# Kernel tuning notes

Measured on AMD Instinct MI355X. Metric: run time of the kernel, lower is better.

Reference implementation:

```python
import jax, jax.numpy as jnp
import numpy as np

D_MODEL = 128
NUM_HEADS = 8
DEPTH = D_MODEL // NUM_HEADS
NEG = -1e9


def _dense_params(key, d_in, d_out):
    kw, kb = jax.random.split(key)
    # Glorot-uniform like keras Dense default
    lim = np.sqrt(6.0 / (d_in + d_out))
    w = jax.random.uniform(kw, (d_in, d_out), jnp.float32, -lim, lim)
    b = jnp.zeros((d_out,), jnp.float32)
    return w, b


def setup_inputs() -> dict:
    key = jax.random.key(0)
    ks = jax.random.split(key, 16)
    B, N, M, d = 256, 128, 128, D_MODEL
    inp = {
        'x_self': jax.random.normal(ks[0], (B, N, d), jnp.float32),
        'adj_self': jax.random.randint(ks[1], (B, N, N), 0, 2, jnp.int32),
        'mask_self': jnp.ones((B, N), jnp.int32),
        'x_cross': jax.random.normal(ks[2], (B, M, d), jnp.float32),
        'mask_cross': jnp.ones((B, M), jnp.int32),
    }
    names = ['wq_s', 'wk_s', 'wv_s', 'wo_s', 'wq_c', 'wk_c', 'wv_c', 'wo_c']
    for i, nm in enumerate(names):
        w, b = _dense_params(ks[3 + i], d, d)
        inp[nm] = w
        inp['b' + nm[1:]] = b
    wg, bg = _dense_params(ks[12], 3 * d, d)
    inp['wg'] = wg
    inp['bg'] = bg
    return inp


def _split_heads(x):
    B, N, _ = x.shape
    return x.reshape(B, N, NUM_HEADS, DEPTH).transpose(0, 2, 1, 3)  # [B,H,N,depth]


def _merge_heads(x):
    B, H, N, Dp = x.shape
    return x.transpose(0, 2, 1, 3).reshape(B, N, H * Dp)


def _attention(q, k, v, mask, adj=None):
    # q,k,v: [B,H,Nq,depth]; mask: [B,Nk]; adj: [B,Nq,Nk] or None
    logits = jnp.einsum('bhqd,bhkd->bhqk', q, k) / jnp.sqrt(jnp.float32(DEPTH))
    if adj is not None:
        logits = logits + ((1.0 - adj.astype(jnp.float32)) * NEG)[:, None, :, :]
    logits = logits + ((1.0 - mask.astype(jnp.float32)) * NEG)[:, None, None, :]
    w = jax.nn.softmax(logits, axis=-1)
    return jnp.einsum('bhqk,bhkd->bhqd', w, v)


def reference(x_self, adj_self, mask_self, x_cross, mask_cross,
              wq_s, bq_s, wk_s, bk_s, wv_s, bv_s, wo_s, bo_s,
              wq_c, bq_c, wk_c, bk_c, wv_c, bv_c, wo_c, bo_c,
              wg, bg):
    # Self attention (adjacency + padding mask)
    q_s = _split_heads(x_self @ wq_s + bq_s)
    k_s = _split_heads(x_self @ wk_s + bk_s)
    v_s = _split_heads(x_self @ wv_s + bv_s)
    out_s = _merge_heads(_attention(q_s, k_s, v_s, mask_self, adj_self)) @ wo_s + bo_s
    # Cross attention (padding mask only); dropout inactive at inference
    q_c = _split_heads(x_self @ wq_c + bq_c)
    k_c = _split_heads(x_cross @ wk_c + bk_c)
    v_c = _split_heads(x_cross @ wv_c + bv_c)
    out_c = _merge_heads(_attention(q_c, k_c, v_c, mask_cross)) @ wo_c + bo_c
    # Sigmoid gate fusion
    gate = jax.nn.sigmoid(jnp.concatenate([x_self, out_s, out_c], axis=-1) @ wg + bg)
    return (1.0 - gate) * out_s + gate * out_c
```

## Files before the change

### kernel.cpp

```cpp
#include <hip/hip_runtime.h>
#include <hip/hip_bf16.h>

typedef _Float16 f16_t;
typedef __attribute__((ext_vector_type(8))) _Float16 f16x8;
typedef __attribute__((ext_vector_type(4))) float f32x4;
typedef __attribute__((ext_vector_type(16))) float f32x16;

__global__ __launch_bounds__(256) void transpose_w(
    const float* w0, const float* w1, const float* w2, const float* w3,
    const float* w4, const float* w5, const float* w6, const float* w7,
    const float* wg, f16_t* wt)
{
  __shared__ float t[128][129];
  const int b = blockIdx.x;
  const int tid = threadIdx.x;
  const float* src;
  f16_t* dst;
  int ostride;
  switch (b) {
    case 0: src = w0; break;  case 1: src = w1; break;
    case 2: src = w2; break;  case 3: src = w3; break;
    case 4: src = w4; break;  case 5: src = w5; break;
    case 6: src = w6; break;  case 7: src = w7; break;
    default: src = wg + (size_t)(b - 8) * 16384; break;
  }
  if (b < 8) { dst = wt + (size_t)b * 16384; ostride = 128; }
  else       { dst = wt + 8 * 16384 + (b - 8) * 128; ostride = 384; }

#pragma unroll
  for (int i = 0; i < 64; ++i) {
    const int idx = tid + i * 256;
    const int r = idx >> 7, c = idx & 127;
    t[c][r] = src[idx];
  }
  __syncthreads();
#pragma unroll
  for (int i = 0; i < 64; ++i) {
    const int idx = tid + i * 256;
    const int c = idx >> 7, r = idx & 127;
    dst[(size_t)c * ostride + r] = (f16_t)t[c][r];
  }
}

template <int NW>
__global__ __launch_bounds__(256) void projN_kernel(
    const float* __restrict__ A, const f16_t* __restrict__ WT,
    const float* __restrict__ bias0, f16_t* __restrict__ Y0,
    const float* __restrict__ bias1, f16_t* __restrict__ Y1,
    const float* __restrict__ bias2, f16_t* __restrict__ Y2,
    const float* __restrict__ bias3, f16_t* __restrict__ Y3)
{
  const int tid = threadIdx.x;
  const int wv = tid >> 6;
  const int ln = tid & 63;
  const int l15 = ln & 15;
  const int g = ln >> 4;
  const size_t arow = (size_t)blockIdx.x * 64 + wv * 16 + l15;

  f32x4 acc[NW][8];
#pragma unroll
  for (int i = 0; i < NW; ++i)
#pragma unroll
    for (int nt = 0; nt < 8; ++nt) acc[i][nt] = (f32x4){0.f, 0.f, 0.f, 0.f};

#pragma unroll
  for (int kt = 0; kt < 4; ++kt) {
    const float* ap = A + arow * 128 + kt * 32 + g * 8;
    float4 v0 = *(const float4*)ap;
    float4 v1 = *(const float4*)(ap + 4);
    f16x8 a;
    a[0] = (f16_t)v0.x; a[1] = (f16_t)v0.y; a[2] = (f16_t)v0.z; a[3] = (f16_t)v0.w;
    a[4] = (f16_t)v1.x; a[5] = (f16_t)v1.y; a[6] = (f16_t)v1.z; a[7] = (f16_t)v1.w;
#pragma unroll
    for (int i = 0; i < NW; ++i) {
#pragma unroll
      for (int nt = 0; nt < 8; ++nt) {
        f16x8 b = *(const f16x8*)(WT + (size_t)i * 16384 +
                                  (size_t)(nt * 16 + l15) * 128 + kt * 32 + g * 8);
        acc[i][nt] = __builtin_amdgcn_mfma_f32_16x16x32_f16(a, b, acc[i][nt], 0, 0, 0);
      }
    }
  }

  const size_t orow0 = (size_t)blockIdx.x * 64 + wv * 16 + g * 4;
#pragma unroll
  for (int i = 0; i < NW; ++i) {
    const float* bp = (i == 0) ? bias0 : (i == 1) ? bias1 : (i == 2) ? bias2 : bias3;
    f16_t* Y = (i == 0) ? Y0 : (i == 1) ? Y1 : (i == 2) ? Y2 : Y3;
#pragma unroll
    for (int nt = 0; nt < 8; ++nt) {
      const int col = nt * 16 + l15;
      const float bv = bp[col];
#pragma unroll
      for (int r = 0; r < 4; ++r)
        Y[(orow0 + r) * 128 + col] = (f16_t)(acc[i][nt][r] + bv);
    }
  }
}

template <bool HAS_ADJ>
__global__ __launch_bounds__(256) void attn3_kernel(
    const f16_t* __restrict__ Q, const f16_t* __restrict__ K,
    const f16_t* __restrict__ V, const int* __restrict__ adj,
    const int* __restrict__ mask, f16_t* __restrict__ O)
{
  __shared__ __align__(16) f16_t Qh[128 * 24];
  __shared__ __align__(16) f16_t Kh[128 * 24];
  __shared__ __align__(16) f16_t Vt[16 * 136];
  __shared__ __align__(16) f16_t Pl[128 * 128];
  __shared__ float larr[128];
  __shared__ unsigned mw[4];
  __shared__ unsigned adjw[HAS_ADJ ? 128 * 4 : 4];

  const int bid = blockIdx.x;
  const int h = bid >> 8;
  const int bb = bid & 255;
  const int tid = threadIdx.x;
  const size_t base = (size_t)bb * 16384 + h * 16;

  {
    const int r = tid >> 1, hf = tid & 1;
    f16x8 qv = *(const f16x8*)(Q + base + (size_t)r * 128 + hf * 8);
    *(f16x8*)&Qh[r * 24 + hf * 8] = qv;
    f16x8 kv = *(const f16x8*)(K + base + (size_t)r * 128 + hf * 8);
    *(f16x8*)&Kh[r * 24 + hf * 8] = kv;
    f16x8 vv = *(const f16x8*)(V + base + (size_t)r * 128 + hf * 8);
#pragma unroll
    for (int j = 0; j < 8; ++j) Vt[(hf * 8 + j) * 136 + r] = vv[j];
  }
  if (tid < 128) {
    unsigned long long bm = __ballot(mask[bb * 128 + tid] != 0);
    if ((tid & 63) == 0) {
      mw[(tid >> 6) * 2 + 0] = (unsigned)bm;
      mw[(tid >> 6) * 2 + 1] = (unsigned)(bm >> 32);
    }
  }
  if (HAS_ADJ) {
    const int r = tid >> 1, hf = tid & 1;
    const int4* ap = (const int4*)(adj + ((size_t)bb * 128 + r) * 128 + hf * 64);
    unsigned w0 = 0, w1 = 0;
#pragma unroll
    for (int i = 0; i < 8; ++i) {
      int4 a = ap[i];
      unsigned m4 = (a.x != 0 ? 1u : 0u) | (a.y != 0 ? 2u : 0u) |
                    (a.z != 0 ? 4u : 0u) | (a.w != 0 ? 8u : 0u);
      w0 |= m4 << (i * 4);
    }
#pragma unroll
    for (int i = 8; i < 16; ++i) {
      int4 a = ap[i];
      unsigned m4 = (a.x != 0 ? 1u : 0u) | (a.y != 0 ? 2u : 0u) |
                    (a.z != 0 ? 4u : 0u) | (a.w != 0 ? 8u : 0u);
      w1 |= m4 << ((i - 8) * 4);
    }
    adjw[r * 4 + hf * 2 + 0] = w0;
    adjw[r * 4 + hf * 2 + 1] = w1;
  }
  __syncthreads();

  const int ln = tid & 63;
  const int wv = tid >> 6;
  const int l31 = ln & 31;
  const int hh = ln >> 5;
  const int q = wv * 32 + l31;

  f32x16 zero16;
#pragma unroll
  for (int j = 0; j < 16; ++j) zero16[j] = 0.f;
  const f16x8 bq = *(const f16x8*)&Qh[q * 24 + hh * 8];
  f32x16 st[4];
#pragma unroll
  for (int kt = 0; kt < 4; ++kt) {
    const f16x8 ak = *(const f16x8*)&Kh[(kt * 32 + l31) * 24 + hh * 8];
    st[kt] = __builtin_amdgcn_mfma_f32_32x32x16_f16(ak, bq, zero16, 0, 0, 0);
  }

  unsigned aw[4];
#pragma unroll
  for (int kt = 0; kt < 4; ++kt)
    aw[kt] = HAS_ADJ ? (adjw[q * 4 + kt] & mw[kt]) : mw[kt];

  const int swz = (q & 7) << 4;
  float l = 0.f;
#pragma unroll
  for (int kt = 0; kt < 4; ++kt) {
#pragma unroll
    for (int r2 = 0; r2 < 8; ++r2) {
      const int r = r2 * 2;
      const int koff = (r & 3) + 8 * (r >> 2) + 4 * hh;
      float e0 = __expf(st[kt][r]     * 0.25f - 8.f);
      float e1 = __expf(st[kt][r + 1] * 0.25f - 8.f);
      float p0 = ((aw[kt] >> koff) & 1u) ? e0 : 0.f;
      float p1 = ((aw[kt] >> (koff + 1)) & 1u) ? e1 : 0.f;
      l += p0 + p1;
      unsigned short u0 = __builtin_bit_cast(unsigned short, (f16_t)p0);
      unsigned short u1 = __builtin_bit_cast(unsigned short, (f16_t)p1);
      unsigned pk = (unsigned)u0 | ((unsigned)u1 << 16);
      const int key = kt * 32 + koff;
      *(unsigned*)((char*)Pl + q * 256 + ((key * 2) ^ swz)) = pk;
    }
  }
  l += __shfl_xor(l, 32);
  if (hh == 0) larr[q] = l;
  __syncthreads();

  const int l15 = ln & 15;
  const int g4 = ln >> 4;
  const int qa0 = wv * 32 + l15;
  const int qa1 = qa0 + 16;
  const int swz0 = (qa0 & 7) << 4;
  const int swz1 = (qa1 & 7) << 4;
  f32x4 o0 = (f32x4){0.f, 0.f, 0.f, 0.f};
  f32x4 o1 = (f32x4){0.f, 0.f, 0.f, 0.f};
#pragma unroll
  for (int kt = 0; kt < 4; ++kt) {
    const f16x8 bv = *(const f16x8*)&Vt[l15 * 136 + kt * 32 + g4 * 8];
    const f16x8 p0 = *(const f16x8*)((char*)Pl + qa0 * 256 + ((kt * 64 + g4 * 16) ^ swz0));
    const f16x8 p1 = *(const f16x8*)((char*)Pl + qa1 * 256 + ((kt * 64 + g4 * 16) ^ swz1));
    o0 = __builtin_amdgcn_mfma_f32_16x16x32_f16(p0, bv, o0, 0, 0, 0);
    o1 = __builtin_amdgcn_mfma_f32_16x16x32_f16(p1, bv, o1, 0, 0, 0);
  }
#pragma unroll
  for (int rr = 0; rr < 4; ++rr) {
    const int q0 = wv * 32 + g4 * 4 + rr;
    const int q1 = q0 + 16;
    const float i0 = 1.f / larr[q0];
    const float i1 = 1.f / larr[q1];
    O[base + (size_t)q0 * 128 + l15] = (f16_t)(o0[rr] * i0);
    O[base + (size_t)q1 * 128 + l15] = (f16_t)(o1[rr] * i1);
  }
}

__global__ __launch_bounds__(256) void outgate_kernel(
    const f16_t* __restrict__ AS, const f16_t* __restrict__ AC,
    const float* __restrict__ X, const f16_t* __restrict__ WT,
    const float* __restrict__ bos, const float* __restrict__ boc,
    const float* __restrict__ bgv, float* __restrict__ OUT)
{
  __shared__ __align__(16) f16_t OSl[64 * 136];
  __shared__ __align__(16) f16_t OCl[64 * 136];
  const int tid = threadIdx.x;
  const int wv = tid >> 6;
  const int ln = tid & 63;
  const int l15 = ln & 15;
  const int g = ln >> 4;
  const size_t arow = (size_t)blockIdx.x * 64 + wv * 16 + l15;
  const f16_t* WoS = WT + 6 * 16384;
  const f16_t* WoC = WT + 7 * 16384;
  const f16_t* Wg  = WT + 8 * 16384;

  f32x4 accS[8], accC[8], accG[8];
#pragma unroll
  for (int nt = 0; nt < 8; ++nt) {
    accS[nt] = (f32x4){0.f, 0.f, 0.f, 0.f};
    accC[nt] = (f32x4){0.f, 0.f, 0.f, 0.f};
    accG[nt] = (f32x4){0.f, 0.f, 0.f, 0.f};
  }

#pragma unroll
  for (int kt = 0; kt < 4; ++kt) {
    f16x8 aS = *(const f16x8*)(AS + arow * 128 + kt * 32 + g * 8);
    f16x8 aC = *(const f16x8*)(AC + arow * 128 + kt * 32 + g * 8);
#pragma unroll
    for (int nt = 0; nt < 8; ++nt) {
      f16x8 bS = *(const f16x8*)(WoS + (size_t)(nt * 16 + l15) * 128 + kt * 32 + g * 8);
      f16x8 bC = *(const f16x8*)(WoC + (size_t)(nt * 16 + l15) * 128 + kt * 32 + g * 8);
      accS[nt] = __builtin_amdgcn_mfma_f32_16x16x32_f16(aS, bS, accS[nt], 0, 0, 0);
      accC[nt] = __builtin_amdgcn_mfma_f32_16x16x32_f16(aC, bC, accC[nt], 0, 0, 0);
    }
  }
  const int lrow0 = wv * 16 + g * 4;
#pragma unroll
  for (int nt = 0; nt < 8; ++nt) {
    const int col = nt * 16 + l15;
    const float bS = bos[col], bC = boc[col];
#pragma unroll
    for (int r = 0; r < 4; ++r) {
      accS[nt][r] += bS;
      accC[nt][r] += bC;
      OSl[(lrow0 + r) * 136 + col] = (f16_t)accS[nt][r];
      OCl[(lrow0 + r) * 136 + col] = (f16_t)accC[nt][r];
    }
  }
  __syncthreads();

#pragma unroll
  for (int kt = 0; kt < 12; ++kt) {
    f16x8 a;
    if (kt < 4) {
      const float* ap = X + arow * 128 + kt * 32 + g * 8;
      float4 v0 = *(const float4*)ap;
      float4 v1 = *(const float4*)(ap + 4);
      a[0] = (f16_t)v0.x; a[1] = (f16_t)v0.y; a[2] = (f16_t)v0.z; a[3] = (f16_t)v0.w;
      a[4] = (f16_t)v1.x; a[5] = (f16_t)v1.y; a[6] = (f16_t)v1.z; a[7] = (f16_t)v1.w;
    } else if (kt < 8) {
      a = *(const f16x8*)&OSl[(wv * 16 + l15) * 136 + (kt - 4) * 32 + g * 8];
    } else {
      a = *(const f16x8*)&OCl[(wv * 16 + l15) * 136 + (kt - 8) * 32 + g * 8];
    }
#pragma unroll
    for (int nt = 0; nt < 8; ++nt) {
      f16x8 b = *(const f16x8*)(Wg + (size_t)(nt * 16 + l15) * 384 + kt * 32 + g * 8);
      accG[nt] = __builtin_amdgcn_mfma_f32_16x16x32_f16(a, b, accG[nt], 0, 0, 0);
    }
  }

  const size_t orow0 = (size_t)blockIdx.x * 64 + wv * 16 + g * 4;
#pragma unroll
  for (int nt = 0; nt < 8; ++nt) {
    const int col = nt * 16 + l15;
    const float bgc = bgv[col];
#pragma unroll
    for (int r = 0; r < 4; ++r) {
      const float gv = 1.f / (1.f + __expf(-(accG[nt][r] + bgc)));
      OUT[(orow0 + r) * 128 + col] = (1.f - gv) * accS[nt][r] + gv * accC[nt][r];
    }
  }
}

extern "C" void kernel_launch(void* const* d_in, const int* in_sizes, int n_in,
                              void* d_out, int out_size, void* d_ws, size_t ws_size,
                              hipStream_t stream)
{
  const float* x_self  = (const float*)d_in[0];
  const int*   adj     = (const int*)d_in[1];
  const int*   mask_s  = (const int*)d_in[2];
  const float* x_cross = (const float*)d_in[3];
  const int*   mask_c  = (const int*)d_in[4];
  const float* wq_s = (const float*)d_in[5];
  const float* bq_s = (const float*)d_in[6];
  const float* wk_s = (const float*)d_in[7];
  const float* bk_s = (const float*)d_in[8];
  const float* wv_s = (const float*)d_in[9];
  const float* bv_s = (const float*)d_in[10];
  const float* wo_s = (const float*)d_in[11];
  const float* bo_s = (const float*)d_in[12];
  const float* wq_c = (const float*)d_in[13];
  const float* bq_c = (const float*)d_in[14];
  const float* wk_c = (const float*)d_in[15];
  const float* bk_c = (const float*)d_in[16];
  const float* wv_c = (const float*)d_in[17];
  const float* bv_c = (const float*)d_in[18];
  const float* wo_c = (const float*)d_in[19];
  const float* bo_c = (const float*)d_in[20];
  const float* wg   = (const float*)d_in[21];
  const float* bg   = (const float*)d_in[22];
  float* out = (float*)d_out;

  const size_t SZ = (size_t)256 * 128 * 128;
  f16_t* w16 = (f16_t*)d_ws;
  f16_t* qs  = w16 + 0 * SZ;
  f16_t* ks  = w16 + 1 * SZ;
  f16_t* vs  = w16 + 2 * SZ;
  f16_t* qc  = w16 + 3 * SZ;
  f16_t* kc  = w16 + 4 * SZ;
  f16_t* vc  = w16 + 5 * SZ;
  f16_t* as_ = w16 + 6 * SZ;
  f16_t* ac_ = w16 + 7 * SZ;
  f16_t* WT  = w16 + 8 * SZ;

  transpose_w<<<11, 256, 0, stream>>>(wq_s, wk_s, wv_s, wq_c, wk_c, wv_c,
                                      wo_s, wo_c, wg, WT);
  projN_kernel<4><<<512, 256, 0, stream>>>(x_self, WT,
                                           bq_s, qs, bk_s, ks, bv_s, vs, bq_c, qc);
  projN_kernel<2><<<512, 256, 0, stream>>>(x_cross, WT + 4 * 16384,
                                           bk_c, kc, bv_c, vc, nullptr, nullptr,
                                           nullptr, nullptr);
  attn3_kernel<true><<<2048, 256, 0, stream>>>(qs, ks, vs, adj, mask_s, as_);
  attn3_kernel<false><<<2048, 256, 0, stream>>>(qc, kc, vc, nullptr, mask_c, ac_);
  outgate_kernel<<<512, 256, 0, stream>>>(as_, ac_, x_self, WT, bo_s, bo_c, bg, out);
}
```

Baseline: 162.8 us.

## Merge launches, precompose gate weights, and split projection tiles by columns

The two projection launches become one 2048-block launch and the two attention launches become one 4096-block launch, with a block-index switch selecting self or cross inputs. A prep kernel precomputes Wo_s·Wg and Wo_c·Wg plus a folded gate bias. This lets the output kernel compute the gate directly from the attention outputs, dropping the LDS staging, barrier and second GEMM pass. Projection and output tiles shrink to 32 rows with warps split across column halves, doubling the block count. The precomposed weights add fp16 rounding of a product matrix and some extra MFMA work per output block.

```diff
diff --git a/kernel.cpp b/kernel.cpp
--- a/kernel.cpp
+++ b/kernel.cpp
@@ -6,90 +6,133 @@
 typedef __attribute__((ext_vector_type(4))) float f32x4;
 typedef __attribute__((ext_vector_type(16))) float f32x16;
 
-__global__ __launch_bounds__(256) void transpose_w(
-    const float* w0, const float* w1, const float* w2, const float* w3,
-    const float* w4, const float* w5, const float* w6, const float* w7,
-    const float* wg, f16_t* wt)
-{
-  __shared__ float t[128][129];
+__device__ __forceinline__ f16x8 cvt8(const float* p) {
+  float4 v0 = *(const float4*)p;
+  float4 v1 = *(const float4*)(p + 4);
+  f16x8 a;
+  a[0] = (f16_t)v0.x; a[1] = (f16_t)v0.y; a[2] = (f16_t)v0.z; a[3] = (f16_t)v0.w;
+  a[4] = (f16_t)v1.x; a[5] = (f16_t)v1.y; a[6] = (f16_t)v1.z; a[7] = (f16_t)v1.w;
+  return a;
+}
+
+__global__ __launch_bounds__(256) void prep_kernel(
+    const float* wq_s, const float* wk_s, const float* wv_s,
+    const float* wq_c, const float* wk_c, const float* wv_c,
+    const float* wo_s, const float* wo_c, const float* wg,
+    const float* bos, const float* boc, const float* bgin,
+    f16_t* WT, float* bgp)
+{
   const int b = blockIdx.x;
   const int tid = threadIdx.x;
-  const float* src;
-  f16_t* dst;
-  int ostride;
-  switch (b) {
-    case 0: src = w0; break;  case 1: src = w1; break;
-    case 2: src = w2; break;  case 3: src = w3; break;
-    case 4: src = w4; break;  case 5: src = w5; break;
-    case 6: src = w6; break;  case 7: src = w7; break;
-    default: src = wg + (size_t)(b - 8) * 16384; break;
-  }
-  if (b < 8) { dst = wt + (size_t)b * 16384; ostride = 128; }
-  else       { dst = wt + 8 * 16384 + (b - 8) * 128; ostride = 384; }
-
-#pragma unroll
-  for (int i = 0; i < 64; ++i) {
-    const int idx = tid + i * 256;
-    const int r = idx >> 7, c = idx & 127;
-    t[c][r] = src[idx];
-  }
-  __syncthreads();
-#pragma unroll
-  for (int i = 0; i < 64; ++i) {
-    const int idx = tid + i * 256;
-    const int c = idx >> 7, r = idx & 127;
-    dst[(size_t)c * ostride + r] = (f16_t)t[c][r];
+  if (b < 11) {
+    __shared__ float t[128][129];
+    const float* src; f16_t* dst; int ostride;
+    switch (b) {
+      case 0: src = wq_s; break; case 1: src = wk_s; break;
+      case 2: src = wv_s; break; case 3: src = wq_c; break;
+      case 4: src = wk_c; break; case 5: src = wv_c; break;
+      case 6: src = wo_s; break; case 7: src = wo_c; break;
+      default: src = wg + (size_t)(b - 8) * 16384; break;
+    }
+    if (b < 8) { dst = WT + (size_t)b * 16384; ostride = 128; }
+    else       { dst = WT + 8 * 16384 + (b - 8) * 128; ostride = 384; }
+#pragma unroll
+    for (int i = 0; i < 64; ++i) {
+      const int idx = tid + i * 256;
+      t[idx & 127][idx >> 7] = src[idx];
+    }
+    __syncthreads();
+#pragma unroll
+    for (int i = 0; i < 64; ++i) {
+      const int idx = tid + i * 256;
+      const int c = idx >> 7, r = idx & 127;
+      dst[(size_t)c * ostride + r] = (f16_t)t[c][r];
+    }
+  } else if (b < 13) {
+    const int matsel = b - 11;
+    const float* wo = matsel ? wo_c : wo_s;
+    const int joff = 128 + matsel * 128;
+    f16_t* dst = WT + (size_t)(11 + matsel) * 16384;
+    const int wv = tid >> 6, ln = tid & 63, l15 = ln & 15, g = ln >> 4;
+    f32x4 acc[2][8];
+#pragma unroll
+    for (int mm = 0; mm < 2; ++mm)
+#pragma unroll
+      for (int nt = 0; nt < 8; ++nt) acc[mm][nt] = (f32x4){0.f, 0.f, 0.f, 0.f};
+#pragma unroll
+    for (int kt = 0; kt < 4; ++kt) {
+      f16x8 a[2];
+#pragma unroll
+      for (int mm = 0; mm < 2; ++mm) {
+        const int crow = wv * 32 + mm * 16 + l15;
+#pragma unroll
+        for (int jj = 0; jj < 8; ++jj)
+          a[mm][jj] = (f16_t)wg[(size_t)(joff + kt * 32 + g * 8 + jj) * 128 + crow];
+      }
+#pragma unroll
+      for (int nt = 0; nt < 8; ++nt) {
+        f16x8 bf = cvt8(wo + (size_t)(nt * 16 + l15) * 128 + kt * 32 + g * 8);
+        acc[0][nt] = __builtin_amdgcn_mfma_f32_16x16x32_f16(a[0], bf, acc[0][nt], 0, 0, 0);
+        acc[1][nt] = __builtin_amdgcn_mfma_f32_16x16x32_f16(a[1], bf, acc[1][nt], 0, 0, 0);
+      }
+    }
+#pragma unroll
+    for (int mm = 0; mm < 2; ++mm)
+#pragma unroll
+      for (int nt = 0; nt < 8; ++nt)
+#pragma unroll
+        for (int r = 0; r < 4; ++r) {
+          const int c = wv * 32 + mm * 16 + g * 4 + r;
+          dst[(size_t)c * 128 + nt * 16 + l15] = (f16_t)acc[mm][nt][r];
+        }
+  } else {
+    if (tid < 128) {
+      float acc = bgin[tid];
+      for (int j = 0; j < 128; ++j)
+        acc += bos[j] * wg[(size_t)(128 + j) * 128 + tid] +
+               boc[j] * wg[(size_t)(256 + j) * 128 + tid];
+      bgp[tid] = acc;
+    }
   }
 }
 
 template <int NW>
-__global__ __launch_bounds__(256) void projN_kernel(
-    const float* __restrict__ A, const f16_t* __restrict__ WT,
-    const float* __restrict__ bias0, f16_t* __restrict__ Y0,
-    const float* __restrict__ bias1, f16_t* __restrict__ Y1,
-    const float* __restrict__ bias2, f16_t* __restrict__ Y2,
-    const float* __restrict__ bias3, f16_t* __restrict__ Y3)
-{
-  const int tid = threadIdx.x;
-  const int wv = tid >> 6;
-  const int ln = tid & 63;
-  const int l15 = ln & 15;
-  const int g = ln >> 4;
-  const size_t arow = (size_t)blockIdx.x * 64 + wv * 16 + l15;
-
-  f32x4 acc[NW][8];
+__device__ __forceinline__ void proj_body(
+    const float* __restrict__ A, const f16_t* __restrict__ WT, int blk, int tid,
+    const float* b0, f16_t* Y0, const float* b1, f16_t* Y1,
+    const float* b2, f16_t* Y2, const float* b3, f16_t* Y3)
+{
+  const int wv = tid >> 6, ln = tid & 63, l15 = ln & 15, g = ln >> 4;
+  const int rowgrp = wv & 1, colgrp = wv >> 1;
+  const size_t arow = (size_t)blk * 32 + rowgrp * 16 + l15;
+
+  f32x4 acc[NW][4];
 #pragma unroll
   for (int i = 0; i < NW; ++i)
 #pragma unroll
-    for (int nt = 0; nt < 8; ++nt) acc[i][nt] = (f32x4){0.f, 0.f, 0.f, 0.f};
+    for (int nt = 0; nt < 4; ++nt) acc[i][nt] = (f32x4){0.f, 0.f, 0.f, 0.f};
 
 #pragma unroll
   for (int kt = 0; kt < 4; ++kt) {
-    const float* ap = A + arow * 128 + kt * 32 + g * 8;
-    float4 v0 = *(const float4*)ap;
-    float4 v1 = *(const float4*)(ap + 4);
-    f16x8 a;
-    a[0] = (f16_t)v0.x; a[1] = (f16_t)v0.y; a[2] = (f16_t)v0.z; a[3] = (f16_t)v0.w;
-    a[4] = (f16_t)v1.x; a[5] = (f16_t)v1.y; a[6] = (f16_t)v1.z; a[7] = (f16_t)v1.w;
-#pragma unroll
-    for (int i = 0; i < NW; ++i) {
-#pragma unroll
-      for (int nt = 0; nt < 8; ++nt) {
-        f16x8 b = *(const f16x8*)(WT + (size_t)i * 16384 +
-                                  (size_t)(nt * 16 + l15) * 128 + kt * 32 + g * 8);
-        acc[i][nt] = __builtin_amdgcn_mfma_f32_16x16x32_f16(a, b, acc[i][nt], 0, 0, 0);
+    f16x8 a = cvt8(A + arow * 128 + kt * 32 + g * 8);
+#pragma unroll
+    for (int i = 0; i < NW; ++i)
+#pragma unroll
+      for (int nt = 0; nt < 4; ++nt) {
+        f16x8 bfr = *(const f16x8*)(WT + (size_t)i * 16384 +
+                     (size_t)(colgrp * 64 + nt * 16 + l15) * 128 + kt * 32 + g * 8);
+        acc[i][nt] = __builtin_amdgcn_mfma_f32_16x16x32_f16(a, bfr, acc[i][nt], 0, 0, 0);
       }
-    }
-  }
-
-  const size_t orow0 = (size_t)blockIdx.x * 64 + wv * 16 + g * 4;
+  }
+
+  const size_t orow0 = (size_t)blk * 32 + rowgrp * 16 + g * 4;
 #pragma unroll
   for (int i = 0; i < NW; ++i) {
-    const float* bp = (i == 0) ? bias0 : (i == 1) ? bias1 : (i == 2) ? bias2 : bias3;
+    const float* bp = (i == 0) ? b0 : (i == 1) ? b1 : (i == 2) ? b2 : b3;
     f16_t* Y = (i == 0) ? Y0 : (i == 1) ? Y1 : (i == 2) ? Y2 : Y3;
 #pragma unroll
-    for (int nt = 0; nt < 8; ++nt) {
-      const int col = nt * 16 + l15;
+    for (int nt = 0; nt < 4; ++nt) {
+      const int col = colgrp * 64 + nt * 16 + l15;
       const float bv = bp[col];
 #pragma unroll
       for (int r = 0; r < 4; ++r)
@@ -98,11 +141,28 @@
   }
 }
 
-template <bool HAS_ADJ>
-__global__ __launch_bounds__(256) void attn3_kernel(
-    const f16_t* __restrict__ Q, const f16_t* __restrict__ K,
-    const f16_t* __restrict__ V, const int* __restrict__ adj,
-    const int* __restrict__ mask, f16_t* __restrict__ O)
+__global__ __launch_bounds__(256) void projall_kernel(
+    const float* __restrict__ Xs, const float* __restrict__ Xc,
+    const f16_t* __restrict__ WT,
+    const float* bq_s, const float* bk_s, const float* bv_s, const float* bq_c,
+    const float* bk_c, const float* bv_c,
+    f16_t* qs, f16_t* ks, f16_t* vs, f16_t* qc, f16_t* kc, f16_t* vc)
+{
+  if (blockIdx.x < 1024)
+    proj_body<4>(Xs, WT, blockIdx.x, threadIdx.x,
+                 bq_s, qs, bk_s, ks, bv_s, vs, bq_c, qc);
+  else
+    proj_body<2>(Xc, WT + 4 * 16384, blockIdx.x - 1024, threadIdx.x,
+                 bk_c, kc, bv_c, vc, nullptr, nullptr, nullptr, nullptr);
+}
+
+__global__ __launch_bounds__(256) void attn4_kernel(
+    const f16_t* __restrict__ Qs, const f16_t* __restrict__ Ks,
+    const f16_t* __restrict__ Vs, f16_t* __restrict__ Os,
+    const f16_t* __restrict__ Qc, const f16_t* __restrict__ Kc,
+    const f16_t* __restrict__ Vc, f16_t* __restrict__ Oc,
+    const int* __restrict__ adj, const int* __restrict__ mask_s,
+    const int* __restrict__ mask_c)
 {
   __shared__ __align__(16) f16_t Qh[128 * 24];
   __shared__ __align__(16) f16_t Kh[128 * 24];
@@ -110,13 +170,19 @@
   __shared__ __align__(16) f16_t Pl[128 * 128];
   __shared__ float larr[128];
   __shared__ unsigned mw[4];
-  __shared__ unsigned adjw[HAS_ADJ ? 128 * 4 : 4];
-
-  const int bid = blockIdx.x;
+  __shared__ unsigned adjw[128 * 4];
+
+  const bool self = blockIdx.x < 2048;
+  const int bid = blockIdx.x & 2047;
   const int h = bid >> 8;
   const int bb = bid & 255;
   const int tid = threadIdx.x;
   const size_t base = (size_t)bb * 16384 + h * 16;
+  const f16_t* Q = self ? Qs : Qc;
+  const f16_t* K = self ? Ks : Kc;
+  const f16_t* V = self ? Vs : Vc;
+  f16_t* O = self ? Os : Oc;
+  const int* mask = self ? mask_s : mask_c;
 
   {
     const int r = tid >> 1, hf = tid & 1;
@@ -135,7 +201,7 @@
       mw[(tid >> 6) * 2 + 1] = (unsigned)(bm >> 32);
     }
   }
-  if (HAS_ADJ) {
+  if (self) {
     const int r = tid >> 1, hf = tid & 1;
     const int4* ap = (const int4*)(adj + ((size_t)bb * 128 + r) * 128 + hf * 64);
     unsigned w0 = 0, w1 = 0;
@@ -178,7 +244,7 @@
   unsigned aw[4];
 #pragma unroll
   for (int kt = 0; kt < 4; ++kt)
-    aw[kt] = HAS_ADJ ? (adjw[q * 4 + kt] & mw[kt]) : mw[kt];
+    aw[kt] = self ? (adjw[q * 4 + kt] & mw[kt]) : mw[kt];
 
   const int swz = (q & 7) << 4;
   float l = 0.f;
@@ -224,34 +290,30 @@
   for (int rr = 0; rr < 4; ++rr) {
     const int q0 = wv * 32 + g4 * 4 + rr;
     const int q1 = q0 + 16;
-    const float i0 = 1.f / larr[q0];
-    const float i1 = 1.f / larr[q1];
-    O[base + (size_t)q0 * 128 + l15] = (f16_t)(o0[rr] * i0);
-    O[base + (size_t)q1 * 128 + l15] = (f16_t)(o1[rr] * i1);
-  }
-}
-
-__global__ __launch_bounds__(256) void outgate_kernel(
+    O[base + (size_t)q0 * 128 + l15] = (f16_t)(o0[rr] / larr[q0]);
+    O[base + (size_t)q1 * 128 + l15] = (f16_t)(o1[rr] / larr[q1]);
+  }
+}
+
+__global__ __launch_bounds__(256) void outgate2_kernel(
     const f16_t* __restrict__ AS, const f16_t* __restrict__ AC,
     const float* __restrict__ X, const f16_t* __restrict__ WT,
     const float* __restrict__ bos, const float* __restrict__ boc,
-    const float* __restrict__ bgv, float* __restrict__ OUT)
-{
-  __shared__ __align__(16) f16_t OSl[64 * 136];
-  __shared__ __align__(16) f16_t OCl[64 * 136];
+    const float* __restrict__ bgp, float* __restrict__ OUT)
+{
   const int tid = threadIdx.x;
-  const int wv = tid >> 6;
-  const int ln = tid & 63;
-  const int l15 = ln & 15;
-  const int g = ln >> 4;
-  const size_t arow = (size_t)blockIdx.x * 64 + wv * 16 + l15;
+  const int wv = tid >> 6, ln = tid & 63, l15 = ln & 15, g = ln >> 4;
+  const int rowgrp = wv & 1, colgrp = wv >> 1;
+  const size_t arow = (size_t)blockIdx.x * 32 + rowgrp * 16 + l15;
   const f16_t* WoS = WT + 6 * 16384;
   const f16_t* WoC = WT + 7 * 16384;
-  const f16_t* Wg  = WT + 8 * 16384;
-
-  f32x4 accS[8], accC[8], accG[8];
-#pragma unroll
-  for (int nt = 0; nt < 8; ++nt) {
+  const f16_t* WgT = WT + 8 * 16384;
+  const f16_t* W2T = WT + 11 * 16384;
+  const f16_t* W3T = WT + 12 * 16384;
+
+  f32x4 accS[4], accC[4], accG[4];
+#pragma unroll
+  for (int nt = 0; nt < 4; ++nt) {
     accS[nt] = (f32x4){0.f, 0.f, 0.f, 0.f};
     accC[nt] = (f32x4){0.f, 0.f, 0.f, 0.f};
     accG[nt] = (f32x4){0.f, 0.f, 0.f, 0.f};
@@ -259,61 +321,37 @@
 
 #pragma unroll
   for (int kt = 0; kt < 4; ++kt) {
-    f16x8 aS = *(const f16x8*)(AS + arow * 128 + kt * 32 + g * 8);
-    f16x8 aC = *(const f16x8*)(AC + arow * 128 + kt * 32 + g * 8);
-#pragma unroll
-    for (int nt = 0; nt < 8; ++nt) {
-      f16x8 bS = *(const f16x8*)(WoS + (size_t)(nt * 16 + l15) * 128 + kt * 32 + g * 8);
-      f16x8 bC = *(const f16x8*)(WoC + (size_t)(nt * 16 + l15) * 128 + kt * 32 + g * 8);
+    const size_t ko = kt * 32 + g * 8;
+    f16x8 aS = *(const f16x8*)(AS + arow * 128 + ko);
+    f16x8 aC = *(const f16x8*)(AC + arow * 128 + ko);
+    f16x8 aX = cvt8(X + arow * 128 + ko);
+#pragma unroll
+    for (int nt = 0; nt < 4; ++nt) {
+      const size_t col = colgrp * 64 + nt * 16 + l15;
+      f16x8 bS = *(const f16x8*)(WoS + col * 128 + ko);
+      f16x8 bC = *(const f16x8*)(WoC + col * 128 + ko);
+      f16x8 b2 = *(const f16x8*)(W2T + col * 128 + ko);
+      f16x8 b3 = *(const f16x8*)(W3T + col * 128 + ko);
+      f16x8 bX = *(const f16x8*)(WgT + col * 384 + ko);
       accS[nt] = __builtin_amdgcn_mfma_f32_16x16x32_f16(aS, bS, accS[nt], 0, 0, 0);
       accC[nt] = __builtin_amdgcn_mfma_f32_16x16x32_f16(aC, bC, accC[nt], 0, 0, 0);
-    }
-  }
-  const int lrow0 = wv * 16 + g * 4;
-#pragma unroll
-  for (int nt = 0; nt < 8; ++nt) {
-    const int col = nt * 16 + l15;
-    const float bS = bos[col], bC = boc[col];
+      accG[nt] = __builtin_amdgcn_mfma_f32_16x16x32_f16(aX, bX, accG[nt], 0, 0, 0);
+      accG[nt] = __builtin_amdgcn_mfma_f32_16x16x32_f16(aS, b2, accG[nt], 0, 0, 0);
+      accG[nt] = __builtin_amdgcn_mfma_f32_16x16x32_f16(aC, b3, accG[nt], 0, 0, 0);
+    }
+  }
+
+  const size_t orow0 = (size_t)blockIdx.x * 32 + rowgrp * 16 + g * 4;
+#pragma unroll
+  for (int nt = 0; nt < 4; ++nt) {
+    const int col = colgrp * 64 + nt * 16 + l15;
+    const float bS = bos[col], bC = boc[col], bG = bgp[col];
 #pragma unroll
     for (int r = 0; r < 4; ++r) {
-      accS[nt][r] += bS;
-      accC[nt][r] += bC;
-      OSl[(lrow0 + r) * 136 + col] = (f16_t)accS[nt][r];
-      OCl[(lrow0 + r) * 136 + col] = (f16_t)accC[nt][r];
-    }
-  }
-  __syncthreads();
-
-#pragma unroll
-  for (int kt = 0; kt < 12; ++kt) {
-    f16x8 a;
-    if (kt < 4) {
-      const float* ap = X + arow * 128 + kt * 32 + g * 8;
-      float4 v0 = *(const float4*)ap;
-      float4 v1 = *(const float4*)(ap + 4);
-      a[0] = (f16_t)v0.x; a[1] = (f16_t)v0.y; a[2] = (f16_t)v0.z; a[3] = (f16_t)v0.w;
-      a[4] = (f16_t)v1.x; a[5] = (f16_t)v1.y; a[6] = (f16_t)v1.z; a[7] = (f16_t)v1.w;
-    } else if (kt < 8) {
-      a = *(const f16x8*)&OSl[(wv * 16 + l15) * 136 + (kt - 4) * 32 + g * 8];
-    } else {
-      a = *(const f16x8*)&OCl[(wv * 16 + l15) * 136 + (kt - 8) * 32 + g * 8];
-    }
-#pragma unroll
-    for (int nt = 0; nt < 8; ++nt) {
-      f16x8 b = *(const f16x8*)(Wg + (size_t)(nt * 16 + l15) * 384 + kt * 32 + g * 8);
-      accG[nt] = __builtin_amdgcn_mfma_f32_16x16x32_f16(a, b, accG[nt], 0, 0, 0);
-    }
-  }
-
-  const size_t orow0 = (size_t)blockIdx.x * 64 + wv * 16 + g * 4;
-#pragma unroll
-  for (int nt = 0; nt < 8; ++nt) {
-    const int col = nt * 16 + l15;
-    const float bgc = bgv[col];
-#pragma unroll
-    for (int r = 0; r < 4; ++r) {
-      const float gv = 1.f / (1.f + __expf(-(accG[nt][r] + bgc)));
-      OUT[(orow0 + r) * 128 + col] = (1.f - gv) * accS[nt][r] + gv * accC[nt][r];
+      const float os = accS[nt][r] + bS;
+      const float oc = accC[nt][r] + bC;
+      const float gv = 1.f / (1.f + __expf(-(accG[nt][r] + bG)));
+      OUT[(orow0 + r) * 128 + col] = (1.f - gv) * os + gv * oc;
     }
   }
 }
@@ -358,15 +396,15 @@
   f16_t* as_ = w16 + 6 * SZ;
   f16_t* ac_ = w16 + 7 * SZ;
   f16_t* WT  = w16 + 8 * SZ;
-
-  transpose_w<<<11, 256, 0, stream>>>(wq_s, wk_s, wv_s, wq_c, wk_c, wv_c,
-                                      wo_s, wo_c, wg, WT);
-  projN_kernel<4><<<512, 256, 0, stream>>>(x_self, WT,
-                                           bq_s, qs, bk_s, ks, bv_s, vs, bq_c, qc);
-  projN_kernel<2><<<512, 256, 0, stream>>>(x_cross, WT + 4 * 16384,
-                                           bk_c, kc, bv_c, vc, nullptr, nullptr,
-                                           nullptr, nullptr);
-  attn3_kernel<true><<<2048, 256, 0, stream>>>(qs, ks, vs, adj, mask_s, as_);
-  attn3_kernel<false><<<2048, 256, 0, stream>>>(qc, kc, vc, nullptr, mask_c, ac_);
-  outgate_kernel<<<512, 256, 0, stream>>>(as_, ac_, x_self, WT, bo_s, bo_c, bg, out);
-}
+  float* bgp = (float*)(WT + 13 * 16384);
+
+  prep_kernel<<<14, 256, 0, stream>>>(wq_s, wk_s, wv_s, wq_c, wk_c, wv_c,
+                                      wo_s, wo_c, wg, bo_s, bo_c, bg, WT, bgp);
+  projall_kernel<<<2048, 256, 0, stream>>>(x_self, x_cross, WT,
+                                           bq_s, bk_s, bv_s, bq_c, bk_c, bv_c,
+                                           qs, ks, vs, qc, kc, vc);
+  attn4_kernel<<<4096, 256, 0, stream>>>(qs, ks, vs, as_, qc, kc, vc, ac_,
+                                         adj, mask_s, mask_c);
+  outgate2_kernel<<<1024, 256, 0, stream>>>(as_, ac_, x_self, WT,
+                                            bo_s, bo_c, bgp, out);
+}
```

Measured after the change: 159.2 us. 2.2% less time.
